# Optimization experiments

Measured on AMD Instinct MI355X. Metric: run time of the kernel, lower is better.

Reference implementation:

```python
import jax, jax.numpy as jnp
import numpy as np

K = 3
LAST_DIM = 128
IM_H, IM_W = 1024.0, 1536.0
CROP = 2 * K  # tf.image.crop_and_resize crop size [2k, 2k]


def crop_and_resize(image, boxes, box_ids, crop_size):
    """Faithful port of tf.image.crop_and_resize (bilinear, extrapolation=0).
    image: (B,H,W,C); boxes: (N,4) normalized [y1,x1,y2,x2]; box_ids: (N,) int32.
    Returns (N, S, S, C)."""
    H, W = image.shape[1], image.shape[2]
    S = crop_size
    y1, x1, y2, x2 = boxes[:, 0], boxes[:, 1], boxes[:, 2], boxes[:, 3]
    s = jnp.arange(S, dtype=boxes.dtype)
    # sampling coordinates (S > 1 branch of TF)
    ys = y1[:, None] * (H - 1) + s[None, :] * ((y2 - y1)[:, None] * (H - 1) / (S - 1))  # (N,S)
    xs = x1[:, None] * (W - 1) + s[None, :] * ((x2 - x1)[:, None] * (W - 1) / (S - 1))  # (N,S)
    valid_y = (ys >= 0) & (ys <= H - 1)
    valid_x = (xs >= 0) & (xs <= W - 1)
    y0f = jnp.floor(ys)
    x0f = jnp.floor(xs)
    ly = ys - y0f  # bilinear fractions
    lx = xs - x0f
    y0i = jnp.clip(y0f.astype(jnp.int32), 0, H - 1)
    y1i = jnp.clip(y0i + 1, 0, H - 1)
    x0i = jnp.clip(x0f.astype(jnp.int32), 0, W - 1)
    x1i = jnp.clip(x0i + 1, 0, W - 1)
    b = box_ids[:, None, None]

    def g(yi, xi):
        # gather (N,S,S,C) corner values
        return image[b, yi[:, :, None], xi[:, None, :]]

    lx_b = lx[:, None, :, None]
    top = g(y0i, x0i) * (1 - lx_b) + g(y0i, x1i) * lx_b
    bot = g(y1i, x0i) * (1 - lx_b) + g(y1i, x1i) * lx_b
    ly_b = ly[:, :, None, None]
    out = top * (1 - ly_b) + bot * ly_b
    mask = (valid_y[:, :, None] & valid_x[:, None, :]).astype(out.dtype)[..., None]
    return out * mask


def setup_inputs() -> dict:
    key = jax.random.key(0)
    k_feat, k_bid, k_xy, k_wh = jax.random.split(key, 4)
    B, H, W = 4, 64, 96
    N = 2048
    feature_maps = jax.random.normal(k_feat, (B, H, W, K * K * LAST_DIM), dtype=jnp.float32)
    batch_ids = jax.random.randint(k_bid, (N,), 0, B).astype(jnp.float32)
    # top-left corners in image coords, plausible box sizes
    xy = jax.random.uniform(k_xy, (N, 2), dtype=jnp.float32)
    wh = jax.random.uniform(k_wh, (N, 2), dtype=jnp.float32)
    x1 = xy[:, 0] * (0.7 * IM_W)
    y1 = xy[:, 1] * (0.7 * IM_H)
    x2 = x1 + 32.0 + wh[:, 0] * (0.3 * IM_W - 32.0)
    y2 = y1 + 32.0 + wh[:, 1] * (0.3 * IM_H - 32.0)
    rois = jnp.stack([batch_ids, x1, y1, x2, y2], axis=-1)
    return {"feature_maps": feature_maps, "rois": rois}


def reference(feature_maps, rois):
    k = K
    rois = rois.reshape(-1, 5)
    batch_ids = rois[:, 0].astype(jnp.int32)
    norm = jnp.array([IM_W, IM_H, IM_W, IM_H], dtype=rois.dtype)
    bx = rois[:, 1:] / norm                                   # x1,y1,x2,y2 normalized
    boxes = jnp.stack([bx[:, 1], bx[:, 0], bx[:, 3], bx[:, 2]], axis=-1)  # y1,x1,y2,x2
    bin_w = (boxes[:, 3] - boxes[:, 1]) / k
    bin_h = boxes[:, 2] - boxes[:, 0] / k  # faithful bug: missing parens in original
    C = feature_maps.shape[-1] // (k * k)
    acc = 0.0
    for ih in range(k):
        for iw in range(k):
            idx = ih * k + iw
            # faithful bug: fourth coordinate uses bin_h instead of bin_w
            box = jnp.stack([
                boxes[:, 0] + ih * bin_h,
                boxes[:, 1] + iw * bin_w,
                boxes[:, 0] + (ih + 1) * bin_h,
                boxes[:, 1] + (iw + 1) * bin_h,
            ], axis=-1)
            feat = feature_maps[..., idx * C:(idx + 1) * C]
            acc = acc + crop_and_resize(feat, box, batch_ids, CROP)
    sensitive = acc / (k * k)           # (N, 2k, 2k, C)
    out = jnp.mean(sensitive, axis=(1, 2))  # (N, C)
    return out[None]                    # (1, N, C)
```

## Files before the change

kernel.cpp:

```cpp
#include <hip/hip_runtime.h>

constexpr int   CC      = 128;
constexpr int   WSTRIDE = 9 * 128;
constexpr int   HSTRIDE = 96 * WSTRIDE;
constexpr long  BSTRIDE = 64L * HSTRIDE;

__device__ __forceinline__ void box_setup(const float* __restrict__ rois,
                                          int n, int wid,
                                          int& b, float& ybase, float& ystep,
                                          float& xbase, float& xstep) {
  const float r0  = rois[n * 5 + 0];
  const float rx1 = rois[n * 5 + 1];
  const float ry1 = rois[n * 5 + 2];
  const float rx2 = rois[n * 5 + 3];
  const float ry2 = rois[n * 5 + 4];
  b = (int)r0;

  const float x1 = rx1 / 1536.0f;
  const float y1 = ry1 / 1024.0f;
  const float x2 = rx2 / 1536.0f;
  const float y2 = ry2 / 1024.0f;

  const float bin_w = (x2 - x1) / 3.0f;
  const float bin_h = y2 - y1 / 3.0f;

  const int ih = wid / 3;
  const int iw = wid - 3 * ih;

  const float by1 = y1 + (float)ih * bin_h;
  const float bx1 = x1 + (float)iw * bin_w;
  const float by2 = y1 + (float)(ih + 1) * bin_h;
  const float bx2 = x1 + (float)(iw + 1) * bin_h;

  ystep = ((by2 - by1) * 63.0f) / 5.0f;
  xstep = ((bx2 - bx1) * 95.0f) / 5.0f;
  ybase = by1 * 63.0f;
  xbase = bx1 * 95.0f;
}

__device__ __forceinline__ void subbox_accum4(const float* __restrict__ feat,
                                              const float* __restrict__ rois,
                                              int n, int wid, int lane,
                                              float4& acc) {
  int b; float ybase, ystep, xbase, xstep;
  box_setup(rois, n, wid, b, ybase, ystep, xbase, xstep);

  const int half = lane >> 5;
  const int cl   = lane & 31;

  int   xo0[3], xo1[3];
  float lx[3], mx[3];
#pragma unroll
  for (int k = 0; k < 3; ++k) {
    const float xs = xbase + (float)(2 * k + half) * xstep;
    mx[k] = (xs >= 0.0f && xs <= 95.0f) ? 1.0f : 0.0f;
    const float xf = floorf(xs);
    lx[k] = xs - xf;
    int xi = (int)xf;
    xi = xi < 0 ? 0 : (xi > 95 ? 95 : xi);
    const int xj = (xi + 1 > 95) ? 95 : xi + 1;
    xo0[k] = xi * WSTRIDE;
    xo1[k] = xj * WSTRIDE;
  }

  const float* fb = feat + (size_t)b * BSTRIDE + wid * CC + 4 * cl;

#pragma unroll
  for (int sy = 0; sy < 6; ++sy) {
    const float ys = ybase + (float)sy * ystep;
    if (!((ys >= 0.0f) && (ys <= 63.0f))) continue;
    const float yf = floorf(ys);
    const float ly = ys - yf;
    int yi = (int)yf;
    yi = yi < 0 ? 0 : (yi > 63 ? 63 : yi);
    const int yj = (yi + 1 > 63) ? 63 : yi + 1;
    const float* row0 = fb + (size_t)yi * HSTRIDE;
    const float* row1 = fb + (size_t)yj * HSTRIDE;

    float4 v00[3], v01[3], v10[3], v11[3];
#pragma unroll
    for (int k = 0; k < 3; ++k) {
      v00[k] = *(const float4*)(row0 + xo0[k]);
      v01[k] = *(const float4*)(row0 + xo1[k]);
      v10[k] = *(const float4*)(row1 + xo0[k]);
      v11[k] = *(const float4*)(row1 + xo1[k]);
    }
#pragma unroll
    for (int k = 0; k < 3; ++k) {
      const float l = lx[k], m = mx[k];
      const float t0 = v00[k].x * (1.0f - l) + v01[k].x * l;
      const float t1 = v00[k].y * (1.0f - l) + v01[k].y * l;
      const float t2 = v00[k].z * (1.0f - l) + v01[k].z * l;
      const float t3 = v00[k].w * (1.0f - l) + v01[k].w * l;
      const float u0 = v10[k].x * (1.0f - l) + v11[k].x * l;
      const float u1 = v10[k].y * (1.0f - l) + v11[k].y * l;
      const float u2 = v10[k].z * (1.0f - l) + v11[k].z * l;
      const float u3 = v10[k].w * (1.0f - l) + v11[k].w * l;
      acc.x += m * (t0 * (1.0f - ly) + u0 * ly);
      acc.y += m * (t1 * (1.0f - ly) + u1 * ly);
      acc.z += m * (t2 * (1.0f - ly) + u2 * ly);
      acc.w += m * (t3 * (1.0f - ly) + u3 * ly);
    }
  }
}

__global__ __launch_bounds__(1024)
void rroi_sort_kernel(const float* __restrict__ rois, int* __restrict__ order,
                      int N) {
  __shared__ unsigned s[2048];
  const int t = threadIdx.x;
  for (int i = t; i < 2048; i += 1024) {
    unsigned key;
    if (i < N) {
      const int   bi = (int)rois[i * 5 + 0];
      const float cx = (rois[i * 5 + 1] + rois[i * 5 + 3]) * 0.5f * (96.0f / 1536.0f);
      const float cy = (rois[i * 5 + 2] + rois[i * 5 + 4]) * 0.5f * (64.0f / 1024.0f);
      int cyi = (int)cy; cyi = cyi < 0 ? 0 : (cyi > 63 ? 63 : cyi);
      int cxi = (int)cx; cxi = cxi < 0 ? 0 : (cxi > 95 ? 95 : cxi);
      key = (unsigned)((bi * 64 + cyi) * 96 + cxi);
    } else {
      key = 0xFFFFFu;
    }
    s[i] = (key << 11) | (unsigned)i;
  }
  __syncthreads();
  for (int k = 2; k <= 2048; k <<= 1) {
    for (int j = k >> 1; j > 0; j >>= 1) {
      for (int i = t; i < 2048; i += 1024) {
        const int ixj = i ^ j;
        if (ixj > i) {
          const unsigned a = s[i], b = s[ixj];
          const bool up = (i & k) == 0;
          if ((a > b) == up) { s[i] = b; s[ixj] = a; }
        }
      }
      __syncthreads();
    }
  }
  for (int i = t; i < 2048; i += 1024)
    if (i < N) order[i] = (int)(s[i] & 0x7FFu);
}

__global__ __launch_bounds__(256)
void rroi_partial_kernel(const float* __restrict__ feat,
                         const float* __restrict__ rois,
                         const int* __restrict__ order,
                         float* __restrict__ ws, int N, int chunk) {
  const int wv    = threadIdx.x >> 6;
  const int lane  = threadIdx.x & 63;
  const int local = (blockIdx.x >> 3) * 4 + wv;
  if (local >= chunk) return;
  const int j = (int)(blockIdx.x & 7) * chunk + local;
  const int total = N * 9;
  if (j >= total) return;
  const int wid  = j / N;
  const int rank = j - wid * N;
  const int n    = order[rank];

  float4 acc = make_float4(0.f, 0.f, 0.f, 0.f);
  subbox_accum4(feat, rois, n, wid, lane, acc);

  acc.x += __shfl_xor(acc.x, 32, 64);
  acc.y += __shfl_xor(acc.y, 32, 64);
  acc.z += __shfl_xor(acc.z, 32, 64);
  acc.w += __shfl_xor(acc.w, 32, 64);

  if ((lane >> 5) == 0) {
    float* p = ws + ((size_t)n * 9 + wid) * CC + 4 * (lane & 31);
    *(float4*)p = acc;
  }
}

__global__ __launch_bounds__(512)
void rroi_reduce_kernel(const float* __restrict__ ws,
                        float* __restrict__ out, int N) {
  const int n = blockIdx.x * 4 + (threadIdx.x >> 7);
  if (n >= N) return;
  const int c = threadIdx.x & 127;
  const float* p = ws + (size_t)n * 9 * CC + c;
  float s = 0.0f;
#pragma unroll
  for (int w = 0; w < 9; ++w) s += p[w * CC];
  out[(size_t)n * CC + c] = s * (1.0f / 324.0f);
}

__global__ __launch_bounds__(576)
void rroi_pool_kernel(const float* __restrict__ feat,
                      const float* __restrict__ rois,
                      float* __restrict__ out, int N) {
  const int n = blockIdx.x;
  const int wid  = threadIdx.x >> 6;
  const int lane = threadIdx.x & 63;
  __shared__ float partial[9][CC];

  float4 acc = make_float4(0.f, 0.f, 0.f, 0.f);
  subbox_accum4(feat, rois, n, wid, lane, acc);

  acc.x += __shfl_xor(acc.x, 32, 64);
  acc.y += __shfl_xor(acc.y, 32, 64);
  acc.z += __shfl_xor(acc.z, 32, 64);
  acc.w += __shfl_xor(acc.w, 32, 64);

  if ((lane >> 5) == 0) {
    const int cl = lane & 31;
    partial[wid][4 * cl + 0] = acc.x;
    partial[wid][4 * cl + 1] = acc.y;
    partial[wid][4 * cl + 2] = acc.z;
    partial[wid][4 * cl + 3] = acc.w;
  }
  __syncthreads();

  if (threadIdx.x < CC) {
    float s = 0.0f;
#pragma unroll
    for (int w = 0; w < 9; ++w) s += partial[w][threadIdx.x];
    out[(size_t)n * CC + threadIdx.x] = s * (1.0f / 324.0f);
  }
}

extern "C" void kernel_launch(void* const* d_in, const int* in_sizes, int n_in,
                              void* d_out, int out_size, void* d_ws, size_t ws_size,
                              hipStream_t stream) {
  const float* feat = (const float*)d_in[0];
  const float* rois = (const float*)d_in[1];
  float* out = (float*)d_out;
  const int N = in_sizes[1] / 5;

  const size_t need = (size_t)N * 9 * CC * sizeof(float) + (size_t)N * sizeof(int);
  if (ws_size >= need && N <= 2048) {
    float* ws    = (float*)d_ws;
    int*   order = (int*)(ws + (size_t)N * 9 * CC);
    const int total = N * 9;
    const int chunk = (total + 7) / 8;
    const int blocks = ((chunk + 3) / 4) * 8;
    rroi_sort_kernel<<<1, 1024, 0, stream>>>(rois, order, N);
    rroi_partial_kernel<<<blocks, 256, 0, stream>>>(feat, rois, order, ws, N, chunk);
    rroi_reduce_kernel<<<(N + 3) / 4, 512, 0, stream>>>(ws, out, N);
  } else {
    rroi_pool_kernel<<<N, 576, 0, stream>>>(feat, rois, out, N);
  }
}
```

Measured before the change: 79.59 us.

## Use persistent grid-stride partial kernel and branchless y-sampling with early exit

```diff
diff --git a/kernel.cpp b/kernel.cpp
--- a/kernel.cpp
+++ b/kernel.cpp
@@ -63,19 +63,35 @@
     xo1[k] = xj * WSTRIDE;
   }
 
-  const float* fb = feat + (size_t)b * BSTRIDE + wid * CC + 4 * cl;
-
+  float my[6], lyv[6];
+  int   ro0[6], ro1[6];
+  bool  anyY = false;
 #pragma unroll
   for (int sy = 0; sy < 6; ++sy) {
     const float ys = ybase + (float)sy * ystep;
-    if (!((ys >= 0.0f) && (ys <= 63.0f))) continue;
+    const bool v = (ys >= 0.0f) && (ys <= 63.0f);
+    anyY |= v;
+    my[sy] = v ? 1.0f : 0.0f;
     const float yf = floorf(ys);
-    const float ly = ys - yf;
+    lyv[sy] = ys - yf;
     int yi = (int)yf;
     yi = yi < 0 ? 0 : (yi > 63 ? 63 : yi);
     const int yj = (yi + 1 > 63) ? 63 : yi + 1;
-    const float* row0 = fb + (size_t)yi * HSTRIDE;
-    const float* row1 = fb + (size_t)yj * HSTRIDE;
+    ro0[sy] = yi * HSTRIDE;
+    ro1[sy] = yj * HSTRIDE;
+  }
+
+  if (!anyY) return;
+  if (!__any(mx[0] + mx[1] + mx[2] > 0.0f)) return;
+
+  const float* fb = feat + (size_t)b * BSTRIDE + wid * CC + 4 * cl;
+
+#pragma unroll
+  for (int sy = 0; sy < 6; ++sy) {
+    const float ly  = lyv[sy];
+    const float oly = 1.0f - ly;
+    const float* row0 = fb + ro0[sy];
+    const float* row1 = fb + ro1[sy];
 
     float4 v00[3], v01[3], v10[3], v11[3];
 #pragma unroll
@@ -87,19 +103,21 @@
     }
 #pragma unroll
     for (int k = 0; k < 3; ++k) {
-      const float l = lx[k], m = mx[k];
-      const float t0 = v00[k].x * (1.0f - l) + v01[k].x * l;
-      const float t1 = v00[k].y * (1.0f - l) + v01[k].y * l;
-      const float t2 = v00[k].z * (1.0f - l) + v01[k].z * l;
-      const float t3 = v00[k].w * (1.0f - l) + v01[k].w * l;
-      const float u0 = v10[k].x * (1.0f - l) + v11[k].x * l;
-      const float u1 = v10[k].y * (1.0f - l) + v11[k].y * l;
-      const float u2 = v10[k].z * (1.0f - l) + v11[k].z * l;
-      const float u3 = v10[k].w * (1.0f - l) + v11[k].w * l;
-      acc.x += m * (t0 * (1.0f - ly) + u0 * ly);
-      acc.y += m * (t1 * (1.0f - ly) + u1 * ly);
-      acc.z += m * (t2 * (1.0f - ly) + u2 * ly);
-      acc.w += m * (t3 * (1.0f - ly) + u3 * ly);
+      const float l  = lx[k];
+      const float ol = 1.0f - l;
+      const float m  = mx[k] * my[sy];
+      const float t0 = v00[k].x * ol + v01[k].x * l;
+      const float t1 = v00[k].y * ol + v01[k].y * l;
+      const float t2 = v00[k].z * ol + v01[k].z * l;
+      const float t3 = v00[k].w * ol + v01[k].w * l;
+      const float u0 = v10[k].x * ol + v11[k].x * l;
+      const float u1 = v10[k].y * ol + v11[k].y * l;
+      const float u2 = v10[k].z * ol + v11[k].z * l;
+      const float u3 = v10[k].w * ol + v11[k].w * l;
+      acc.x += m * (t0 * oly + u0 * ly);
+      acc.y += m * (t1 * oly + u1 * ly);
+      acc.z += m * (t2 * oly + u2 * ly);
+      acc.w += m * (t3 * oly + u3 * ly);
     }
   }
 }
@@ -141,33 +159,32 @@
     if (i < N) order[i] = (int)(s[i] & 0x7FFu);
 }
 
-__global__ __launch_bounds__(256)
+__global__ __launch_bounds__(256, 2)
 void rroi_partial_kernel(const float* __restrict__ feat,
                          const float* __restrict__ rois,
                          const int* __restrict__ order,
-                         float* __restrict__ ws, int N, int chunk) {
-  const int wv    = threadIdx.x >> 6;
-  const int lane  = threadIdx.x & 63;
-  const int local = (blockIdx.x >> 3) * 4 + wv;
-  if (local >= chunk) return;
-  const int j = (int)(blockIdx.x & 7) * chunk + local;
+                         float* __restrict__ ws, int N, int W) {
+  const int gw   = blockIdx.x * 4 + (threadIdx.x >> 6);
+  const int lane = threadIdx.x & 63;
   const int total = N * 9;
-  if (j >= total) return;
-  const int wid  = j / N;
-  const int rank = j - wid * N;
-  const int n    = order[rank];
-
-  float4 acc = make_float4(0.f, 0.f, 0.f, 0.f);
-  subbox_accum4(feat, rois, n, wid, lane, acc);
-
-  acc.x += __shfl_xor(acc.x, 32, 64);
-  acc.y += __shfl_xor(acc.y, 32, 64);
-  acc.z += __shfl_xor(acc.z, 32, 64);
-  acc.w += __shfl_xor(acc.w, 32, 64);
-
-  if ((lane >> 5) == 0) {
-    float* p = ws + ((size_t)n * 9 + wid) * CC + 4 * (lane & 31);
-    *(float4*)p = acc;
+
+  for (int j = gw; j < total; j += W) {
+    const int rank = j / 9;
+    const int wid  = j - 9 * rank;
+    const int n    = order[rank];
+
+    float4 acc = make_float4(0.f, 0.f, 0.f, 0.f);
+    subbox_accum4(feat, rois, n, wid, lane, acc);
+
+    acc.x += __shfl_xor(acc.x, 32, 64);
+    acc.y += __shfl_xor(acc.y, 32, 64);
+    acc.z += __shfl_xor(acc.z, 32, 64);
+    acc.w += __shfl_xor(acc.w, 32, 64);
+
+    if ((lane >> 5) == 0) {
+      float* p = ws + ((size_t)n * 9 + wid) * CC + 4 * (lane & 31);
+      *(float4*)p = acc;
+    }
   }
 }
 
@@ -230,11 +247,10 @@
   if (ws_size >= need && N <= 2048) {
     float* ws    = (float*)d_ws;
     int*   order = (int*)(ws + (size_t)N * 9 * CC);
-    const int total = N * 9;
-    const int chunk = (total + 7) / 8;
-    const int blocks = ((chunk + 3) / 4) * 8;
+    const int blocks = 1536;
+    const int W = blocks * 4;
     rroi_sort_kernel<<<1, 1024, 0, stream>>>(rois, order, N);
-    rroi_partial_kernel<<<blocks, 256, 0, stream>>>(feat, rois, order, ws, N, chunk);
+    rroi_partial_kernel<<<blocks, 256, 0, stream>>>(feat, rois, order, ws, N, W);
     rroi_reduce_kernel<<<(N + 3) / 4, 512, 0, stream>>>(ws, out, N);
   } else {
     rroi_pool_kernel<<<N, 576, 0, stream>>>(feat, rois, out, N);
```

Result: slower. 138.2 us (+73.6%).

## Separate bilinear weights and merge duplicate row/column taps to skip redundant loads

Applied to the files above, without the earlier changes.

```diff
diff --git a/kernel.cpp b/kernel.cpp
--- a/kernel.cpp
+++ b/kernel.cpp
@@ -38,69 +38,94 @@
   xbase = bx1 * 95.0f;
 }
 
-__device__ __forceinline__ void subbox_accum4(const float* __restrict__ feat,
-                                              const float* __restrict__ rois,
-                                              int n, int wid, int lane,
-                                              float4& acc) {
+__device__ __forceinline__ void subbox_accum_sep(const float* __restrict__ feat,
+                                                 const float* __restrict__ rois,
+                                                 int n, int wid, int lane,
+                                                 float4& acc) {
   int b; float ybase, ystep, xbase, xstep;
   box_setup(rois, n, wid, b, ybase, ystep, xbase, xstep);
 
   const int half = lane >> 5;
   const int cl   = lane & 31;
 
-  int   xo0[3], xo1[3];
-  float lx[3], mx[3];
-#pragma unroll
-  for (int k = 0; k < 3; ++k) {
-    const float xs = xbase + (float)(2 * k + half) * xstep;
-    mx[k] = (xs >= 0.0f && xs <= 95.0f) ? 1.0f : 0.0f;
-    const float xf = floorf(xs);
-    lx[k] = xs - xf;
-    int xi = (int)xf;
-    xi = xi < 0 ? 0 : (xi > 95 ? 95 : xi);
-    const int xj = (xi + 1 > 95) ? 95 : xi + 1;
-    xo0[k] = xi * WSTRIDE;
-    xo1[k] = xj * WSTRIDE;
-  }
-
-  const float* fb = feat + (size_t)b * BSTRIDE + wid * CC + 4 * cl;
-
-#pragma unroll
-  for (int sy = 0; sy < 6; ++sy) {
-    const float ys = ybase + (float)sy * ystep;
-    if (!((ys >= 0.0f) && (ys <= 63.0f))) continue;
+  float wy[12]; int ry[12];
+#pragma unroll
+  for (int s = 0; s < 6; ++s) {
+    const float ys = ybase + (float)s * ystep;
+    const float m  = (ys >= 0.0f && ys <= 63.0f) ? 1.0f : 0.0f;
     const float yf = floorf(ys);
     const float ly = ys - yf;
     int yi = (int)yf;
     yi = yi < 0 ? 0 : (yi > 63 ? 63 : yi);
     const int yj = (yi + 1 > 63) ? 63 : yi + 1;
-    const float* row0 = fb + (size_t)yi * HSTRIDE;
-    const float* row1 = fb + (size_t)yj * HSTRIDE;
-
-    float4 v00[3], v01[3], v10[3], v11[3];
-#pragma unroll
-    for (int k = 0; k < 3; ++k) {
-      v00[k] = *(const float4*)(row0 + xo0[k]);
-      v01[k] = *(const float4*)(row0 + xo1[k]);
-      v10[k] = *(const float4*)(row1 + xo0[k]);
-      v11[k] = *(const float4*)(row1 + xo1[k]);
-    }
-#pragma unroll
-    for (int k = 0; k < 3; ++k) {
-      const float l = lx[k], m = mx[k];
-      const float t0 = v00[k].x * (1.0f - l) + v01[k].x * l;
-      const float t1 = v00[k].y * (1.0f - l) + v01[k].y * l;
-      const float t2 = v00[k].z * (1.0f - l) + v01[k].z * l;
-      const float t3 = v00[k].w * (1.0f - l) + v01[k].w * l;
-      const float u0 = v10[k].x * (1.0f - l) + v11[k].x * l;
-      const float u1 = v10[k].y * (1.0f - l) + v11[k].y * l;
-      const float u2 = v10[k].z * (1.0f - l) + v11[k].z * l;
-      const float u3 = v10[k].w * (1.0f - l) + v11[k].w * l;
-      acc.x += m * (t0 * (1.0f - ly) + u0 * ly);
-      acc.y += m * (t1 * (1.0f - ly) + u1 * ly);
-      acc.z += m * (t2 * (1.0f - ly) + u2 * ly);
-      acc.w += m * (t3 * (1.0f - ly) + u3 * ly);
-    }
+    ry[2 * s]     = yi; wy[2 * s]     = m * (1.0f - ly);
+    ry[2 * s + 1] = yj; wy[2 * s + 1] = m * ly;
+  }
+#pragma unroll
+  for (int c = 1; c < 12; ++c) {
+    if (ry[c] == ry[c - 1]) { wy[c] += wy[c - 1]; wy[c - 1] = 0.0f; }
+  }
+
+  float wx[6]; int cx[6];
+#pragma unroll
+  for (int k = 0; k < 3; ++k) {
+    const float xs = xbase + (float)(2 * k + half) * xstep;
+    const float m  = (xs >= 0.0f && xs <= 95.0f) ? 1.0f : 0.0f;
+    const float xf = floorf(xs);
+    const float lx = xs - xf;
+    int xi = (int)xf;
+    xi = xi < 0 ? 0 : (xi > 95 ? 95 : xi);
+    const int xj = (xi + 1 > 95) ? 95 : xi + 1;
+    cx[2 * k]     = xi * WSTRIDE; wx[2 * k]     = m * (1.0f - lx);
+    cx[2 * k + 1] = xj * WSTRIDE; wx[2 * k + 1] = m * lx;
+  }
+#pragma unroll
+  for (int c = 1; c < 6; ++c) {
+    if (cx[c] == cx[c - 1]) { wx[c] += wx[c - 1]; wx[c - 1] = 0.0f; }
+  }
+
+  const float* fb = feat + (size_t)b * BSTRIDE + wid * CC + 4 * cl;
+
+#pragma unroll
+  for (int c = 0; c < 12; c += 2) {
+    const bool r0v = (wy[c] != 0.0f);
+    const bool r1v = (wy[c + 1] != 0.0f);
+    if (!r0v && !r1v) continue;
+
+    float4 v0[6], v1[6];
+#pragma unroll
+    for (int k = 0; k < 6; ++k) {
+      v0[k] = make_float4(0.f, 0.f, 0.f, 0.f);
+      v1[k] = make_float4(0.f, 0.f, 0.f, 0.f);
+    }
+    if (r0v) {
+      const float* rp = fb + (size_t)ry[c] * HSTRIDE;
+#pragma unroll
+      for (int k = 0; k < 6; ++k)
+        if (wx[k] != 0.0f) v0[k] = *(const float4*)(rp + cx[k]);
+    }
+    if (r1v) {
+      const float* rp = fb + (size_t)ry[c + 1] * HSTRIDE;
+#pragma unroll
+      for (int k = 0; k < 6; ++k)
+        if (wx[k] != 0.0f) v1[k] = *(const float4*)(rp + cx[k]);
+    }
+
+    float4 ra0 = make_float4(0.f, 0.f, 0.f, 0.f);
+    float4 ra1 = make_float4(0.f, 0.f, 0.f, 0.f);
+#pragma unroll
+    for (int k = 0; k < 6; ++k) {
+      const float w = wx[k];
+      ra0.x += w * v0[k].x; ra0.y += w * v0[k].y;
+      ra0.z += w * v0[k].z; ra0.w += w * v0[k].w;
+      ra1.x += w * v1[k].x; ra1.y += w * v1[k].y;
+      ra1.z += w * v1[k].z; ra1.w += w * v1[k].w;
+    }
+    const float w0 = wy[c], w1 = wy[c + 1];
+    acc.x += w0 * ra0.x + w1 * ra1.x;
+    acc.y += w0 * ra0.y + w1 * ra1.y;
+    acc.z += w0 * ra0.z + w1 * ra1.z;
+    acc.w += w0 * ra0.w + w1 * ra1.w;
   }
 }
 
@@ -158,7 +183,7 @@
   const int n    = order[rank];
 
   float4 acc = make_float4(0.f, 0.f, 0.f, 0.f);
-  subbox_accum4(feat, rois, n, wid, lane, acc);
+  subbox_accum_sep(feat, rois, n, wid, lane, acc);
 
   acc.x += __shfl_xor(acc.x, 32, 64);
   acc.y += __shfl_xor(acc.y, 32, 64);
@@ -194,7 +219,7 @@
   __shared__ float partial[9][CC];
 
   float4 acc = make_float4(0.f, 0.f, 0.f, 0.f);
-  subbox_accum4(feat, rois, n, wid, lane, acc);
+  subbox_accum_sep(feat, rois, n, wid, lane, acc);
 
   acc.x += __shfl_xor(acc.x, 32, 64);
   acc.y += __shfl_xor(acc.y, 32, 64);
```

Result: slower. 90.77 us (+14.1%).
